# Optimization experiments

Measured on AMD Instinct MI355X. Metric: run time of the kernel, lower is better.

Reference implementation:

```python
import jax, jax.numpy as jnp
import numpy as np

N_NODES = 4096
N_EDGES = 65536
BS = 16
LEAKY_SLOPE = 0.01
BN_EPS = 1e-5


def _init(key, shape, scale=0.02):
    return (jax.random.normal(key, shape, dtype=jnp.float32) * scale)


def setup_inputs() -> dict:
    key = jax.random.key(0)
    ks = jax.random.split(key, 20)
    x_in = jax.random.normal(ks[0], (N_NODES, 8500), dtype=jnp.float32)
    edge_index = jax.random.randint(ks[1], (2, N_EDGES), 0, N_NODES, dtype=jnp.int64)
    return {
        "x_in": x_in,
        "edge_index": edge_index,
        # SAGEConv params: Wl (neighbor lin, with bias), Wr (root lin, no bias)
        "W1l": _init(ks[2], (320, 8500)), "b1": jnp.zeros((320,), jnp.float32), "W1r": _init(ks[3], (320, 8500)),
        "W2l": _init(ks[4], (180, 320)),  "b2": jnp.zeros((180,), jnp.float32), "W2r": _init(ks[5], (180, 320)),
        "W3l": _init(ks[6], (90, 180)),   "b3": jnp.zeros((90,), jnp.float32),  "W3r": _init(ks[7], (90, 180)),
        "W4l": _init(ks[8], (50, 90)),    "b4": jnp.zeros((50,), jnp.float32),  "W4r": _init(ks[9], (50, 90)),
        "Wf1": _init(ks[10], (32, 50)),   "bf1": jnp.zeros((32,), jnp.float32),
        "Wf2": _init(ks[11], (16, 32)),   "bf2": jnp.zeros((16,), jnp.float32),
        "Wf3": _init(ks[12], (1, 16)),    "bf3": jnp.zeros((1,), jnp.float32),
    }


def _sage(x, src, dst, Wl, bl, Wr):
    # PyG SAGEConv: out = lin_l(mean_{j in N(i)} x_j) + lin_r(x_i)
    agg = jax.ops.segment_sum(x[src], dst, num_segments=N_NODES)          # [N, F]
    deg = jax.ops.segment_sum(jnp.ones_like(dst, dtype=x.dtype), dst, num_segments=N_NODES)
    mean = agg / jnp.maximum(deg, 1.0)[:, None]
    return mean @ Wl.T + bl + x @ Wr.T


def _leaky(x):
    return jnp.where(x >= 0, x, LEAKY_SLOPE * x)


def _bn(x):
    # F.batch_norm(x, None, None, training=True): per-feature, biased var, no affine
    m = jnp.mean(x, axis=0)
    v = jnp.mean((x - m) ** 2, axis=0)
    return (x - m) / jnp.sqrt(v + BN_EPS)


def reference(x_in, edge_index,
              W1l, b1, W1r, W2l, b2, W2r, W3l, b3, W3r, W4l, b4, W4r,
              Wf1, bf1, Wf2, bf2, Wf3, bf3):
    src, dst = edge_index[0], edge_index[1]
    x = _bn(_leaky(_sage(x_in, src, dst, W1l, b1, W1r)))
    x = _bn(_leaky(_sage(x, src, dst, W2l, b2, W2r)))
    x = _bn(_leaky(_sage(x, src, dst, W3l, b3, W3r)))
    x = _bn(_leaky(_sage(x, src, dst, W4l, b4, W4r)))
    # get_batch: label i -> floor(i / (N/BS)); global_add_pool == segment sum
    x = x.reshape(BS, N_NODES // BS, -1).sum(axis=1)                      # [BS, 50]
    x = x @ Wf1.T + bf1
    x = x @ Wf2.T + bf2
    x = x @ Wf3.T + bf3
    return x
```

## Files before the change

### kernel.cpp

```cpp
#include <hip/hip_runtime.h>
#include <stdint.h>

#define NN 4096
#define NE 65536
#define LEAKY 0.01f
#define BN_EPS 1e-5f
#define DSTRIDE 96

typedef float f32x4 __attribute__((ext_vector_type(4)));
typedef __bf16 bf16x8 __attribute__((ext_vector_type(8)));
typedef unsigned short u16x8 __attribute__((ext_vector_type(8)));

static __device__ __forceinline__ unsigned short f2bf(float v) {
  unsigned int u = __float_as_uint(v);
  u += 0x7fff + ((u >> 16) & 1);
  return (unsigned short)(u >> 16);
}

typedef __attribute__((address_space(1))) void gvoid;
typedef __attribute__((address_space(3))) void lvoid;

static __device__ __forceinline__ void async16(const void* g, void* l) {
  __builtin_amdgcn_global_load_lds((gvoid*)(uintptr_t)g,
                                   (lvoid*)(uint32_t)(uintptr_t)l, 16, 0, 0);
}


static __device__ __forceinline__ void pack_w_seg(int lblk, const float* __restrict__ Wl,
                                                  const float* __restrict__ Wr,
                                                  unsigned short* __restrict__ dst,
                                                  int Fout, int Fin, int Kp, int Np) {
  int nb = Kp >> 3;
  int idx = lblk * 256 + threadIdx.x;
  if (idx >= Np * nb) return;
  int row = idx / nb, kb = idx - row * nb;
  int g = kb >> 3, b = kb & 7;
  int dkb = (g << 3) | ((b + row) & 7);
  const float* src = nullptr;
  if (row < Fout)          src = Wl + (size_t)row * Fin;
  else if (row < 2 * Fout) src = Wr + (size_t)(row - Fout) * Fin;
  u16x8 st;
#pragma unroll
  for (int o = 0; o < 8; ++o) {
    int k = kb * 8 + o;
    float v = (src && k < Fin) ? src[k] : 0.f;
    st[o] = f2bf(v);
  }
  *(u16x8*)&dst[(size_t)row * Kp + dkb * 8] = st;
}

#define PX_BLK   17024
#define PW1_BLK   2660
#define PW2_BLK     60
#define PW3_BLK     24
#define PW4_BLK      8
#define ADJ_BLK    256
#define SETUP_BLK (PX_BLK + PW1_BLK + PW2_BLK + PW3_BLK + PW4_BLK + ADJ_BLK)

__global__ __launch_bounds__(256) void setup_all(
    const float* __restrict__ x, const int* __restrict__ esrc, const int* __restrict__ edst,
    const float* __restrict__ W1l, const float* __restrict__ W1r,
    const float* __restrict__ W2l, const float* __restrict__ W2r,
    const float* __restrict__ W3l, const float* __restrict__ W3r,
    const float* __restrict__ W4l, const float* __restrict__ W4r,
    unsigned short* __restrict__ xbf, unsigned short* __restrict__ wb1,
    unsigned short* __restrict__ wb2, unsigned short* __restrict__ wb3,
    unsigned short* __restrict__ wb4, int* __restrict__ deg, int* __restrict__ eix) {
  int blk = blockIdx.x;
  if (blk < PX_BLK) {
    int idx = blk * 256 + threadIdx.x;
    int row = idx / 1064, kb = idx - row * 1064;
    int g = kb >> 3, b = kb & 7;
    int dkb = (g << 3) | ((b + row) & 7);
    const float* src = x + (size_t)row * 8500 + kb * 8;
    float v[8];
    if (kb < 1062) {
      f32x4 a = *(const f32x4*)src;
      f32x4 c = *(const f32x4*)(src + 4);
#pragma unroll
      for (int o = 0; o < 4; ++o) { v[o] = a[o]; v[o + 4] = c[o]; }
    } else {
#pragma unroll
      for (int o = 0; o < 8; ++o) {
        int k = kb * 8 + o;
        v[o] = (k < 8500) ? x[(size_t)row * 8500 + k] : 0.f;
      }
    }
    u16x8 st;
#pragma unroll
    for (int o = 0; o < 8; ++o) st[o] = f2bf(v[o]);
    *(u16x8*)&xbf[(size_t)row * 8512 + dkb * 8] = st;
  } else if (blk < PX_BLK + PW1_BLK) {
    pack_w_seg(blk - PX_BLK, W1l, W1r, wb1, 320, 8500, 8512, 640);
  } else if (blk < PX_BLK + PW1_BLK + PW2_BLK) {
    pack_w_seg(blk - PX_BLK - PW1_BLK, W2l, W2r, wb2, 180, 320, 320, 384);
  } else if (blk < PX_BLK + PW1_BLK + PW2_BLK + PW3_BLK) {
    pack_w_seg(blk - PX_BLK - PW1_BLK - PW2_BLK, W3l, W3r, wb3, 90, 180, 192, 256);
  } else if (blk < PX_BLK + PW1_BLK + PW2_BLK + PW3_BLK + PW4_BLK) {
    pack_w_seg(blk - PX_BLK - PW1_BLK - PW2_BLK - PW3_BLK, W4l, W4r, wb4, 50, 90, 128, 128);
  } else {
    int e = (blk - (SETUP_BLK - ADJ_BLK)) * 256 + threadIdx.x;
    int d = edst[e];
    int pos = atomicAdd(&deg[d], 1);
    if (pos < DSTRIDE) eix[(size_t)d * DSTRIDE + pos] = esrc[e];
  }
}

__global__ __launch_bounds__(256) void gemm_bt(const unsigned short* __restrict__ A,
                                               const unsigned short* __restrict__ B,
                                               float* __restrict__ C, int N, int K,
                                               int M) {
  __shared__ unsigned short smem[2 * 128 * 64];
  unsigned short* As = smem;
  unsigned short* Bs = smem + 128 * 64;

  const int t = threadIdx.x;
  const int bm = blockIdx.x, bn = blockIdx.y;
  const int lane = t & 63;
  const int wave = t >> 6;
  const int wm = (wave & 1) * 64, wn = (wave >> 1) * 64;
  const int l16 = lane & 15, quad = lane >> 4;

  const int ksteps = K >> 6;
  const int gz = (int)gridDim.z;
  const int per = (ksteps + gz - 1) / gz;
  const int k0 = (int)blockIdx.z * per;
  int k1 = k0 + per; if (k1 > ksteps) k1 = ksteps;

  f32x4 acc[4][4];
#pragma unroll
  for (int i = 0; i < 4; ++i)
#pragma unroll
    for (int j = 0; j < 4; ++j) acc[i][j] = (f32x4){0.f, 0.f, 0.f, 0.f};

  const int srow = t >> 3;
  const int scol = (t & 7) * 8;
  const unsigned short* Abase = A + (size_t)(bm * 128) * K + scol;
  const unsigned short* Bbase = B + (size_t)(bn * 128) * K + scol;

  for (int kt = k0; kt < k1; ++kt) {
    const unsigned short* Ag = Abase + kt * 64;
    const unsigned short* Bg = Bbase + kt * 64;
#pragma unroll
    for (int p = 0; p < 4; ++p) {
      int row = p * 32 + srow;
      async16(Ag + (size_t)row * K, &As[row * 64 + scol]);
    }
#pragma unroll
    for (int p = 0; p < 4; ++p) {
      int row = p * 32 + srow;
      async16(Bg + (size_t)row * K, &Bs[row * 64 + scol]);
    }
    __syncthreads();
#pragma unroll
    for (int kh = 0; kh < 2; ++kh) {
      const int s8 = ((kh * 4 + quad + l16) & 7) * 8;
      bf16x8 af[4], bfr[4];
#pragma unroll
      for (int i = 0; i < 4; ++i)
        af[i] = *(const bf16x8*)&As[(wm + i * 16 + l16) * 64 + s8];
#pragma unroll
      for (int j = 0; j < 4; ++j)
        bfr[j] = *(const bf16x8*)&Bs[(wn + j * 16 + l16) * 64 + s8];
#pragma unroll
      for (int i = 0; i < 4; ++i)
#pragma unroll
        for (int j = 0; j < 4; ++j)
          acc[i][j] = __builtin_amdgcn_mfma_f32_16x16x32_bf16(af[i], bfr[j], acc[i][j], 0, 0, 0);
    }
    __syncthreads();
  }

  float* Cb = C + (size_t)blockIdx.z * M * N;
#pragma unroll
  for (int i = 0; i < 4; ++i) {
    int rbase = bm * 128 + wm + i * 16 + quad * 4;
#pragma unroll
    for (int j = 0; j < 4; ++j) {
      int col = bn * 128 + wn + j * 16 + l16;
      float* cp = Cb + (size_t)rbase * N + col;
#pragma unroll
      for (int r = 0; r < 4; ++r) cp[(size_t)r * N] = acc[i][j][r];
    }
  }
}

__global__ void reduceN(float* __restrict__ y, int nz) {
  int idx = blockIdx.x * 256 + threadIdx.x;
  f32x4* p = (f32x4*)y;
  const int S = NN * 640 / 4;
  f32x4 v = p[idx];
  for (int sl = 1; sl < nz; ++sl) v += p[idx + (size_t)sl * S];
  p[idx] = v;
}

__global__ __launch_bounds__(256) void sage_agg(
    const float* __restrict__ y, const int* __restrict__ deg,
    const int* __restrict__ eix, const float* __restrict__ bias,
    float* __restrict__ z, int F, int ldy) {
  int i = blockIdx.x;
  int tx = threadIdx.x, ty = threadIdx.y;
  int f4 = (blockIdx.y * 64 + tx) * 4;
  __shared__ int se[DSTRIDE];
  __shared__ float red[3][64][4];
  int d = deg[i]; if (d > DSTRIDE) d = DSTRIDE;
  bool active = (f4 < F);
  f32x4 s = {0.f, 0.f, 0.f, 0.f};
  {
    int lt = ty * 64 + tx;
    if (lt < d) se[lt] = eix[(size_t)i * DSTRIDE + lt];
  }
  __syncthreads();
  if (active)
    for (int e = ty; e < d; e += 4)
      s += *(const f32x4*)&y[(size_t)se[e] * ldy + f4];
  if (ty > 0) *(f32x4*)red[ty - 1][tx] = s;
  __syncthreads();
  if (ty == 0 && active) {
    s += *(const f32x4*)red[0][tx];
    s += *(const f32x4*)red[1][tx];
    s += *(const f32x4*)red[2][tx];
    float inv = 1.f / (float)(d > 1 ? d : 1);
    int cnt = F - f4; if (cnt > 4) cnt = 4;
    const float* yr = &y[(size_t)i * ldy + F + f4];
    float* zo = &z[(size_t)i * F + f4];
    for (int j = 0; j < cnt; ++j) {
      float w = s[j] * inv + yr[j] + bias[f4 + j];
      zo[j] = (w >= 0.f) ? w : LEAKY * w;
    }
  }
}


__global__ __launch_bounds__(256) void bn_part(const float* __restrict__ z,
                                               float* __restrict__ sums, int F) {
  int tx = threadIdx.x, ty = threadIdx.y;
  int f = blockIdx.x * 64 + tx;
  float s = 0.f, s2 = 0.f;
  if (f < F) {
    int r0 = blockIdx.y * 512 + ty * 128;
    for (int j = 0; j < 128; ++j) {
      float v = z[(size_t)(r0 + j) * F + f];
      s += v; s2 += v * v;
    }
  }
  __shared__ float ls[4][64], ls2[4][64];
  ls[ty][tx] = s; ls2[ty][tx] = s2;
  __syncthreads();
  if (ty == 0 && f < F) {
    float S  = ls[0][tx] + ls[1][tx] + ls[2][tx] + ls[3][tx];
    float S2 = ls2[0][tx] + ls2[1][tx] + ls2[2][tx] + ls2[3][tx];
    atomicAdd(&sums[f], S);
    atomicAdd(&sums[F + f], S2);
  }
}

__global__ void bn_norm8(const float* __restrict__ z, const float* __restrict__ sums,
                         unsigned short* __restrict__ xout, int F, int Kp) {
  int nb = Kp >> 3;
  int idx = blockIdx.x * 256 + threadIdx.x;
  int row = idx / nb, kb = idx - row * nb;
  int g = kb >> 3, b = kb & 7;
  int dkb = (g << 3) | ((b + row) & 7);
  u16x8 st;
#pragma unroll
  for (int o = 0; o < 8; ++o) {
    int k = kb * 8 + o;
    float v = 0.f;
    if (k < F) {
      float m  = sums[k] * (1.f / NN);
      float var = sums[F + k] * (1.f / NN) - m * m;
      float rs = rsqrtf(var + BN_EPS);
      v = (z[(size_t)row * F + k] - m) * rs;
    }
    st[o] = f2bf(v);
  }
  *(u16x8*)&xout[(size_t)row * Kp + dkb * 8] = st;
}

__global__ void pool_fc(const float* __restrict__ z,
                        const float* __restrict__ sums,
                        const float* __restrict__ Wf1, const float* __restrict__ bf1,
                        const float* __restrict__ Wf2, const float* __restrict__ bf2,
                        const float* __restrict__ Wf3, const float* __restrict__ bf3,
                        float* __restrict__ out) {
  __shared__ float pool[50];
  __shared__ float h1[32], h2[16];
  int b = blockIdx.x, t = threadIdx.x;
  if (t < 50) {
    float s = 0.f;
    for (int r = 0; r < 256; ++r) s += z[(size_t)(b * 256 + r) * 50 + t];
    float m  = sums[t] * (1.f / NN);
    float var = sums[50 + t] * (1.f / NN) - m * m;
    float rs = rsqrtf(var + BN_EPS);
    pool[t] = (s - 256.f * m) * rs;
  }
  __syncthreads();
  if (t < 32) {
    float s = bf1[t];
    for (int f = 0; f < 50; ++f) s += pool[f] * Wf1[t * 50 + f];
    h1[t] = s;
  }
  __syncthreads();
  if (t < 16) {
    float s = bf2[t];
    for (int f = 0; f < 32; ++f) s += h1[f] * Wf2[t * 32 + f];
    h2[t] = s;
  }
  __syncthreads();
  if (t == 0) {
    float s = bf3[0];
    for (int f = 0; f < 16; ++f) s += h2[f] * Wf3[f];
    out[b] = s;
  }
}


extern "C" void kernel_launch(void* const* d_in, const int* in_sizes, int n_in,
                              void* d_out, int out_size, void* d_ws, size_t ws_size,
                              hipStream_t stream) {
  const float* x_in = (const float*)d_in[0];
  const int* ei = (const int*)d_in[1];
  const float* W1l = (const float*)d_in[2];
  const float* b1  = (const float*)d_in[3];
  const float* W1r = (const float*)d_in[4];
  const float* W2l = (const float*)d_in[5];
  const float* b2  = (const float*)d_in[6];
  const float* W2r = (const float*)d_in[7];
  const float* W3l = (const float*)d_in[8];
  const float* b3  = (const float*)d_in[9];
  const float* W3r = (const float*)d_in[10];
  const float* W4l = (const float*)d_in[11];
  const float* b4  = (const float*)d_in[12];
  const float* W4r = (const float*)d_in[13];
  const float* Wf1 = (const float*)d_in[14];
  const float* bf1 = (const float*)d_in[15];
  const float* Wf2 = (const float*)d_in[16];
  const float* bf2 = (const float*)d_in[17];
  const float* Wf3 = (const float*)d_in[18];
  const float* bf3 = (const float*)d_in[19];
  float* out = (float*)d_out;
  (void)in_sizes; (void)n_in; (void)out_size;

  char* ws = (char*)d_ws;
  size_t off = 0;
  auto alloc = [&](size_t bytes) -> void* {
    void* p = ws + off;
    off = (off + bytes + 255) & ~(size_t)255;
    return p;
  };
  unsigned short* xbf = (unsigned short*)alloc((size_t)NN * 8512 * 2);
  unsigned short* wb1 = (unsigned short*)alloc((size_t)640 * 8512 * 2);
  unsigned short* wb2 = (unsigned short*)alloc((size_t)384 * 320 * 2);
  unsigned short* wb3 = (unsigned short*)alloc((size_t)256 * 192 * 2);
  unsigned short* wb4 = (unsigned short*)alloc((size_t)128 * 128 * 2);
  float* z    = (float*)alloc((size_t)NN * 320 * 4);
  int* deg    = (int*)alloc(NN * 4);
  float* bnsum = (float*)alloc(1280 * 4);
  int* eix    = (int*)alloc((size_t)NN * DSTRIDE * 4);
  const size_t YS = (size_t)NN * 640 * 4;
  float* y = (float*)(ws + off);
  int nz = (off + 8 * YS <= ws_size) ? 8 : 4;
  if (off + (size_t)nz * YS > ws_size) return;
  float* bns1 = bnsum;
  float* bns2 = bnsum + 640;
  float* bns3 = bnsum + 1000;
  float* bns4 = bnsum + 1180;

  hipMemsetAsync(deg, 0, NN * 4 + 1280 * 4, stream);

  setup_all<<<dim3(SETUP_BLK), dim3(256), 0, stream>>>(
      x_in, ei, ei + NE, W1l, W1r, W2l, W2r, W3l, W3r, W4l, W4r,
      xbf, wb1, wb2, wb3, wb4, deg, eix);

  gemm_bt<<<dim3(32, 5, nz), dim3(256), 0, stream>>>(xbf, wb1, y, 640, 8512, NN);
  reduceN<<<dim3(NN * 640 / 4 / 256), dim3(256), 0, stream>>>(y, nz);
  sage_agg<<<dim3(NN, 2), dim3(64, 4), 0, stream>>>(y, deg, eix, b1, z, 320, 640);
  bn_part<<<dim3(5, 8), dim3(64, 4), 0, stream>>>(z, bns1, 320);
  bn_norm8<<<dim3(NN * 40 / 256), dim3(256), 0, stream>>>(z, bns1, xbf, 320, 320);

  gemm_bt<<<dim3(32, 3, 1), dim3(256), 0, stream>>>(xbf, wb2, y, 384, 320, NN);
  sage_agg<<<dim3(NN, 1), dim3(64, 4), 0, stream>>>(y, deg, eix, b2, z, 180, 384);
  bn_part<<<dim3(3, 8), dim3(64, 4), 0, stream>>>(z, bns2, 180);
  bn_norm8<<<dim3(NN * 24 / 256), dim3(256), 0, stream>>>(z, bns2, xbf, 180, 192);

  gemm_bt<<<dim3(32, 2, 1), dim3(256), 0, stream>>>(xbf, wb3, y, 256, 192, NN);
  sage_agg<<<dim3(NN, 1), dim3(64, 4), 0, stream>>>(y, deg, eix, b3, z, 90, 256);
  bn_part<<<dim3(2, 8), dim3(64, 4), 0, stream>>>(z, bns3, 90);
  bn_norm8<<<dim3(NN * 16 / 256), dim3(256), 0, stream>>>(z, bns3, xbf, 90, 128);

  gemm_bt<<<dim3(32, 1, 1), dim3(256), 0, stream>>>(xbf, wb4, y, 128, 128, NN);
  sage_agg<<<dim3(NN, 1), dim3(64, 4), 0, stream>>>(y, deg, eix, b4, z, 50, 128);
  bn_part<<<dim3(1, 8), dim3(64, 4), 0, stream>>>(z, bns4, 50);

  pool_fc<<<dim3(16), dim3(64), 0, stream>>>(z, bns4, Wf1, bf1, Wf2, bf2, Wf3, bf3, out);
}
```

Baseline: 511.8 us.

## Pack 64-element groups per thread, loop feature blocks in sage_agg, fix split-K at 4

The bf16 packing of x and the weights now has each thread load 64 floats and write eight swizzled 16-byte chunks, cutting thread count and index math for the large conversion pass. sage_agg handles all feature blocks in one block per node, with a two-way unrolled gather, so the neighbor list is loaded once instead of once per feature block. The first GEMM's split-K is fixed at 4 instead of 8 when workspace allows, which halves the partial-sum buffers reduceN must read. Risks include higher register pressure from the 64-float arrays, and less parallelism in both the first GEMM and the aggregation.

```diff
diff --git a/kernel.cpp b/kernel.cpp
--- a/kernel.cpp
+++ b/kernel.cpp
@@ -26,36 +26,52 @@
 }
 
 
-static __device__ __forceinline__ void pack_w_seg(int lblk, const float* __restrict__ Wl,
-                                                  const float* __restrict__ Wr,
-                                                  unsigned short* __restrict__ dst,
-                                                  int Fout, int Fin, int Kp, int Np) {
-  int nb = Kp >> 3;
+static __device__ __forceinline__ void pack_w_group(int lblk, const float* __restrict__ Wl,
+                                                    const float* __restrict__ Wr,
+                                                    unsigned short* __restrict__ dst,
+                                                    int Fout, int Fin, int Kp, int Np) {
+  int gpr = Kp >> 6;
   int idx = lblk * 256 + threadIdx.x;
-  if (idx >= Np * nb) return;
-  int row = idx / nb, kb = idx - row * nb;
-  int g = kb >> 3, b = kb & 7;
-  int dkb = (g << 3) | ((b + row) & 7);
+  if (idx >= Np * gpr) return;
+  int row = idx / gpr, g = idx - row * gpr;
   const float* src = nullptr;
   if (row < Fout)          src = Wl + (size_t)row * Fin;
   else if (row < 2 * Fout) src = Wr + (size_t)(row - Fout) * Fin;
-  u16x8 st;
-#pragma unroll
-  for (int o = 0; o < 8; ++o) {
-    int k = kb * 8 + o;
-    float v = (src && k < Fin) ? src[k] : 0.f;
-    st[o] = f2bf(v);
-  }
-  *(u16x8*)&dst[(size_t)row * Kp + dkb * 8] = st;
-}
-
-#define PX_BLK   17024
-#define PW1_BLK   2660
-#define PW2_BLK     60
-#define PW3_BLK     24
-#define PW4_BLK      8
-#define ADJ_BLK    256
-#define SETUP_BLK (PX_BLK + PW1_BLK + PW2_BLK + PW3_BLK + PW4_BLK + ADJ_BLK)
+  float v[64];
+  bool al16 = ((Fin & 3) == 0);
+#pragma unroll
+  for (int vv = 0; vv < 16; ++vv) {
+    int k = g * 64 + vv * 4;
+    f32x4 a = (f32x4){0.f, 0.f, 0.f, 0.f};
+    if (src) {
+      if (al16 && k + 4 <= Fin) {
+        a = *(const f32x4*)(src + k);
+      } else {
+#pragma unroll
+        for (int o = 0; o < 4; ++o) a[o] = (k + o < Fin) ? src[k + o] : 0.f;
+      }
+    }
+#pragma unroll
+    for (int o = 0; o < 4; ++o) v[vv * 4 + o] = a[o];
+  }
+  unsigned short* drow = dst + (size_t)row * Kp;
+#pragma unroll
+  for (int b = 0; b < 8; ++b) {
+    int dkb = (g << 3) | ((b + row) & 7);
+    u16x8 st;
+#pragma unroll
+    for (int o = 0; o < 8; ++o) st[o] = f2bf(v[b * 8 + o]);
+    *(u16x8*)&drow[dkb * 8] = st;
+  }
+}
+
+#define PXG_BLK  2128
+#define PW1G      333
+#define PW2G        8
+#define PW3G        3
+#define PW4G        1
+#define ADJ_BLK   256
+#define SETUP_BLK (PXG_BLK + PW1G + PW2G + PW3G + PW4G + ADJ_BLK)
 
 __global__ __launch_bounds__(256) void setup_all(
     const float* __restrict__ x, const int* __restrict__ esrc, const int* __restrict__ edst,
@@ -67,37 +83,36 @@
     unsigned short* __restrict__ wb2, unsigned short* __restrict__ wb3,
     unsigned short* __restrict__ wb4, int* __restrict__ deg, int* __restrict__ eix) {
   int blk = blockIdx.x;
-  if (blk < PX_BLK) {
+  if (blk < PXG_BLK) {
     int idx = blk * 256 + threadIdx.x;
-    int row = idx / 1064, kb = idx - row * 1064;
-    int g = kb >> 3, b = kb & 7;
-    int dkb = (g << 3) | ((b + row) & 7);
-    const float* src = x + (size_t)row * 8500 + kb * 8;
-    float v[8];
-    if (kb < 1062) {
-      f32x4 a = *(const f32x4*)src;
-      f32x4 c = *(const f32x4*)(src + 4);
-#pragma unroll
-      for (int o = 0; o < 4; ++o) { v[o] = a[o]; v[o + 4] = c[o]; }
-    } else {
-#pragma unroll
-      for (int o = 0; o < 8; ++o) {
-        int k = kb * 8 + o;
-        v[o] = (k < 8500) ? x[(size_t)row * 8500 + k] : 0.f;
-      }
-    }
-    u16x8 st;
-#pragma unroll
-    for (int o = 0; o < 8; ++o) st[o] = f2bf(v[o]);
-    *(u16x8*)&xbf[(size_t)row * 8512 + dkb * 8] = st;
-  } else if (blk < PX_BLK + PW1_BLK) {
-    pack_w_seg(blk - PX_BLK, W1l, W1r, wb1, 320, 8500, 8512, 640);
-  } else if (blk < PX_BLK + PW1_BLK + PW2_BLK) {
-    pack_w_seg(blk - PX_BLK - PW1_BLK, W2l, W2r, wb2, 180, 320, 320, 384);
-  } else if (blk < PX_BLK + PW1_BLK + PW2_BLK + PW3_BLK) {
-    pack_w_seg(blk - PX_BLK - PW1_BLK - PW2_BLK, W3l, W3r, wb3, 90, 180, 192, 256);
-  } else if (blk < PX_BLK + PW1_BLK + PW2_BLK + PW3_BLK + PW4_BLK) {
-    pack_w_seg(blk - PX_BLK - PW1_BLK - PW2_BLK - PW3_BLK, W4l, W4r, wb4, 50, 90, 128, 128);
+    int row = idx / 133, g = idx - row * 133;
+    const float* xrow = x + (size_t)row * 8500;
+    float v[64];
+#pragma unroll
+    for (int vv = 0; vv < 16; ++vv) {
+      int k = g * 64 + vv * 4;
+      f32x4 a = (k + 4 <= 8500) ? *(const f32x4*)(xrow + k)
+                                : (f32x4){0.f, 0.f, 0.f, 0.f};
+#pragma unroll
+      for (int o = 0; o < 4; ++o) v[vv * 4 + o] = a[o];
+    }
+    unsigned short* drow = xbf + (size_t)row * 8512;
+#pragma unroll
+    for (int b = 0; b < 8; ++b) {
+      int dkb = (g << 3) | ((b + row) & 7);
+      u16x8 st;
+#pragma unroll
+      for (int o = 0; o < 8; ++o) st[o] = f2bf(v[b * 8 + o]);
+      *(u16x8*)&drow[dkb * 8] = st;
+    }
+  } else if (blk < PXG_BLK + PW1G) {
+    pack_w_group(blk - PXG_BLK, W1l, W1r, wb1, 320, 8500, 8512, 640);
+  } else if (blk < PXG_BLK + PW1G + PW2G) {
+    pack_w_group(blk - PXG_BLK - PW1G, W2l, W2r, wb2, 180, 320, 320, 384);
+  } else if (blk < PXG_BLK + PW1G + PW2G + PW3G) {
+    pack_w_group(blk - PXG_BLK - PW1G - PW2G, W3l, W3r, wb3, 90, 180, 192, 256);
+  } else if (blk < PXG_BLK + PW1G + PW2G + PW3G + PW4G) {
+    pack_w_group(blk - PXG_BLK - PW1G - PW2G - PW3G, W4l, W4r, wb4, 50, 90, 128, 128);
   } else {
     int e = (blk - (SETUP_BLK - ADJ_BLK)) * 256 + threadIdx.x;
     int d = edst[e];
@@ -200,34 +215,45 @@
     float* __restrict__ z, int F, int ldy) {
   int i = blockIdx.x;
   int tx = threadIdx.x, ty = threadIdx.y;
-  int f4 = (blockIdx.y * 64 + tx) * 4;
   __shared__ int se[DSTRIDE];
   __shared__ float red[3][64][4];
   int d = deg[i]; if (d > DSTRIDE) d = DSTRIDE;
-  bool active = (f4 < F);
-  f32x4 s = {0.f, 0.f, 0.f, 0.f};
   {
     int lt = ty * 64 + tx;
     if (lt < d) se[lt] = eix[(size_t)i * DSTRIDE + lt];
   }
   __syncthreads();
-  if (active)
-    for (int e = ty; e < d; e += 4)
-      s += *(const f32x4*)&y[(size_t)se[e] * ldy + f4];
-  if (ty > 0) *(f32x4*)red[ty - 1][tx] = s;
-  __syncthreads();
-  if (ty == 0 && active) {
-    s += *(const f32x4*)red[0][tx];
-    s += *(const f32x4*)red[1][tx];
-    s += *(const f32x4*)red[2][tx];
-    float inv = 1.f / (float)(d > 1 ? d : 1);
-    int cnt = F - f4; if (cnt > 4) cnt = 4;
-    const float* yr = &y[(size_t)i * ldy + F + f4];
-    float* zo = &z[(size_t)i * F + f4];
-    for (int j = 0; j < cnt; ++j) {
-      float w = s[j] * inv + yr[j] + bias[f4 + j];
-      zo[j] = (w >= 0.f) ? w : LEAKY * w;
-    }
+  int nfb = (F + 255) >> 8;
+  for (int fb = 0; fb < nfb; ++fb) {
+    int f4 = (fb * 64 + tx) * 4;
+    bool active = (f4 < F);
+    f32x4 s = {0.f, 0.f, 0.f, 0.f};
+    if (active) {
+      const float* yb = y + f4;
+      int e = ty;
+      for (; e + 4 < d; e += 8) {
+        f32x4 a = *(const f32x4*)&yb[(size_t)se[e] * ldy];
+        f32x4 b = *(const f32x4*)&yb[(size_t)se[e + 4] * ldy];
+        s += a; s += b;
+      }
+      if (e < d) s += *(const f32x4*)&yb[(size_t)se[e] * ldy];
+    }
+    if (ty > 0) *(f32x4*)red[ty - 1][tx] = s;
+    __syncthreads();
+    if (ty == 0 && active) {
+      s += *(const f32x4*)red[0][tx];
+      s += *(const f32x4*)red[1][tx];
+      s += *(const f32x4*)red[2][tx];
+      float inv = 1.f / (float)(d > 1 ? d : 1);
+      int cnt = F - f4; if (cnt > 4) cnt = 4;
+      const float* yr = &y[(size_t)i * ldy + F + f4];
+      float* zo = &z[(size_t)i * F + f4];
+      for (int j = 0; j < cnt; ++j) {
+        float w = s[j] * inv + yr[j] + bias[f4 + j];
+        zo[j] = (w >= 0.f) ? w : LEAKY * w;
+      }
+    }
+    if (fb + 1 < nfb) __syncthreads();
   }
 }
 
@@ -360,7 +386,7 @@
   int* eix    = (int*)alloc((size_t)NN * DSTRIDE * 4);
   const size_t YS = (size_t)NN * 640 * 4;
   float* y = (float*)(ws + off);
-  int nz = (off + 8 * YS <= ws_size) ? 8 : 4;
+  const int nz = 4;
   if (off + (size_t)nz * YS > ws_size) return;
   float* bns1 = bnsum;
   float* bns2 = bnsum + 640;
@@ -375,22 +401,22 @@
 
   gemm_bt<<<dim3(32, 5, nz), dim3(256), 0, stream>>>(xbf, wb1, y, 640, 8512, NN);
   reduceN<<<dim3(NN * 640 / 4 / 256), dim3(256), 0, stream>>>(y, nz);
-  sage_agg<<<dim3(NN, 2), dim3(64, 4), 0, stream>>>(y, deg, eix, b1, z, 320, 640);
+  sage_agg<<<dim3(NN), dim3(64, 4), 0, stream>>>(y, deg, eix, b1, z, 320, 640);
   bn_part<<<dim3(5, 8), dim3(64, 4), 0, stream>>>(z, bns1, 320);
   bn_norm8<<<dim3(NN * 40 / 256), dim3(256), 0, stream>>>(z, bns1, xbf, 320, 320);
 
   gemm_bt<<<dim3(32, 3, 1), dim3(256), 0, stream>>>(xbf, wb2, y, 384, 320, NN);
-  sage_agg<<<dim3(NN, 1), dim3(64, 4), 0, stream>>>(y, deg, eix, b2, z, 180, 384);
+  sage_agg<<<dim3(NN), dim3(64, 4), 0, stream>>>(y, deg, eix, b2, z, 180, 384);
   bn_part<<<dim3(3, 8), dim3(64, 4), 0, stream>>>(z, bns2, 180);
   bn_norm8<<<dim3(NN * 24 / 256), dim3(256), 0, stream>>>(z, bns2, xbf, 180, 192);
 
   gemm_bt<<<dim3(32, 2, 1), dim3(256), 0, stream>>>(xbf, wb3, y, 256, 192, NN);
-  sage_agg<<<dim3(NN, 1), dim3(64, 4), 0, stream>>>(y, deg, eix, b3, z, 90, 256);
+  sage_agg<<<dim3(NN), dim3(64, 4), 0, stream>>>(y, deg, eix, b3, z, 90, 256);
   bn_part<<<dim3(2, 8), dim3(64, 4), 0, stream>>>(z, bns3, 90);
   bn_norm8<<<dim3(NN * 16 / 256), dim3(256), 0, stream>>>(z, bns3, xbf, 90, 128);
 
   gemm_bt<<<dim3(32, 1, 1), dim3(256), 0, stream>>>(xbf, wb4, y, 128, 128, NN);
-  sage_agg<<<dim3(NN, 1), dim3(64, 4), 0, stream>>>(y, deg, eix, b4, z, 50, 128);
+  sage_agg<<<dim3(NN), dim3(64, 4), 0, stream>>>(y, deg, eix, b4, z, 50, 128);
   bn_part<<<dim3(1, 8), dim3(64, 4), 0, stream>>>(z, bns4, 50);
 
   pool_fc<<<dim3(16), dim3(64), 0, stream>>>(z, bns4, Wf1, bf1, Wf2, bf2, Wf3, bf3, out);
```

Measured after the change: 519.1 us. Within noise of the previous version (+1.4%).

## Batch setup conversions, loop feature blocks in aggregation, and fix split-K at four

Applied to the files above, without the earlier changes.

The x-to-bf16 conversion now handles two chunks per thread, so the setup kernel launches half as many of those blocks, and the adjacency-building blocks move to the front so their atomics start early. sage_agg loops over feature blocks inside one block per node instead of using a 2D grid, which loads each node's neighbour list once. Its gather loop is unrolled by two to keep more loads in flight. The split-K depth of the first GEMM is fixed at 4 instead of 8 when workspace allows, which halves the partial buffers and the reduceN traffic but gives the large GEMM fewer blocks to run in parallel.

```diff
diff --git a/kernel.cpp b/kernel.cpp
--- a/kernel.cpp
+++ b/kernel.cpp
@@ -49,13 +49,43 @@
   *(u16x8*)&dst[(size_t)row * Kp + dkb * 8] = st;
 }
 
-#define PX_BLK   17024
-#define PW1_BLK   2660
-#define PW2_BLK     60
-#define PW3_BLK     24
-#define PW4_BLK      8
+static __device__ __forceinline__ void px_load(const float* __restrict__ x, int idx,
+                                               float v[8]) {
+  int row = idx / 1064, kb = idx - row * 1064;
+  const float* src = x + (size_t)row * 8500 + kb * 8;
+  if (kb < 1062) {
+    f32x4 a = *(const f32x4*)src;
+    f32x4 c = *(const f32x4*)(src + 4);
+#pragma unroll
+    for (int o = 0; o < 4; ++o) { v[o] = a[o]; v[o + 4] = c[o]; }
+  } else {
+#pragma unroll
+    for (int o = 0; o < 8; ++o) {
+      int k = kb * 8 + o;
+      v[o] = (k < 8500) ? src[o] : 0.f;
+    }
+  }
+}
+
+static __device__ __forceinline__ void px_store(unsigned short* __restrict__ xbf, int idx,
+                                                const float v[8]) {
+  int row = idx / 1064, kb = idx - row * 1064;
+  int g = kb >> 3, b = kb & 7;
+  int dkb = (g << 3) | ((b + row) & 7);
+  u16x8 st;
+#pragma unroll
+  for (int o = 0; o < 8; ++o) st[o] = f2bf(v[o]);
+  *(u16x8*)&xbf[(size_t)row * 8512 + dkb * 8] = st;
+}
+
 #define ADJ_BLK    256
-#define SETUP_BLK (PX_BLK + PW1_BLK + PW2_BLK + PW3_BLK + PW4_BLK + ADJ_BLK)
+#define PX_HALF  2179072
+#define PX_BLK     8512
+#define PW1_BLK    2660
+#define PW2_BLK      60
+#define PW3_BLK      24
+#define PW4_BLK       8
+#define SETUP_BLK (ADJ_BLK + PX_BLK + PW1_BLK + PW2_BLK + PW3_BLK + PW4_BLK)
 
 __global__ __launch_bounds__(256) void setup_all(
     const float* __restrict__ x, const int* __restrict__ esrc, const int* __restrict__ edst,
@@ -67,42 +97,28 @@
     unsigned short* __restrict__ wb2, unsigned short* __restrict__ wb3,
     unsigned short* __restrict__ wb4, int* __restrict__ deg, int* __restrict__ eix) {
   int blk = blockIdx.x;
-  if (blk < PX_BLK) {
-    int idx = blk * 256 + threadIdx.x;
-    int row = idx / 1064, kb = idx - row * 1064;
-    int g = kb >> 3, b = kb & 7;
-    int dkb = (g << 3) | ((b + row) & 7);
-    const float* src = x + (size_t)row * 8500 + kb * 8;
-    float v[8];
-    if (kb < 1062) {
-      f32x4 a = *(const f32x4*)src;
-      f32x4 c = *(const f32x4*)(src + 4);
-#pragma unroll
-      for (int o = 0; o < 4; ++o) { v[o] = a[o]; v[o + 4] = c[o]; }
-    } else {
-#pragma unroll
-      for (int o = 0; o < 8; ++o) {
-        int k = kb * 8 + o;
-        v[o] = (k < 8500) ? x[(size_t)row * 8500 + k] : 0.f;
-      }
-    }
-    u16x8 st;
-#pragma unroll
-    for (int o = 0; o < 8; ++o) st[o] = f2bf(v[o]);
-    *(u16x8*)&xbf[(size_t)row * 8512 + dkb * 8] = st;
-  } else if (blk < PX_BLK + PW1_BLK) {
-    pack_w_seg(blk - PX_BLK, W1l, W1r, wb1, 320, 8500, 8512, 640);
-  } else if (blk < PX_BLK + PW1_BLK + PW2_BLK) {
-    pack_w_seg(blk - PX_BLK - PW1_BLK, W2l, W2r, wb2, 180, 320, 320, 384);
-  } else if (blk < PX_BLK + PW1_BLK + PW2_BLK + PW3_BLK) {
-    pack_w_seg(blk - PX_BLK - PW1_BLK - PW2_BLK, W3l, W3r, wb3, 90, 180, 192, 256);
-  } else if (blk < PX_BLK + PW1_BLK + PW2_BLK + PW3_BLK + PW4_BLK) {
-    pack_w_seg(blk - PX_BLK - PW1_BLK - PW2_BLK - PW3_BLK, W4l, W4r, wb4, 50, 90, 128, 128);
-  } else {
-    int e = (blk - (SETUP_BLK - ADJ_BLK)) * 256 + threadIdx.x;
+  if (blk < ADJ_BLK) {
+    int e = blk * 256 + threadIdx.x;
     int d = edst[e];
     int pos = atomicAdd(&deg[d], 1);
     if (pos < DSTRIDE) eix[(size_t)d * DSTRIDE + pos] = esrc[e];
+  } else if (blk < ADJ_BLK + PX_BLK) {
+    int idx0 = (blk - ADJ_BLK) * 256 + threadIdx.x;
+    int idx1 = idx0 + PX_HALF;
+    float v0[8], v1[8];
+    px_load(x, idx0, v0);
+    px_load(x, idx1, v1);
+    px_store(xbf, idx0, v0);
+    px_store(xbf, idx1, v1);
+  } else if (blk < ADJ_BLK + PX_BLK + PW1_BLK) {
+    pack_w_seg(blk - ADJ_BLK - PX_BLK, W1l, W1r, wb1, 320, 8500, 8512, 640);
+  } else if (blk < ADJ_BLK + PX_BLK + PW1_BLK + PW2_BLK) {
+    pack_w_seg(blk - ADJ_BLK - PX_BLK - PW1_BLK, W2l, W2r, wb2, 180, 320, 320, 384);
+  } else if (blk < ADJ_BLK + PX_BLK + PW1_BLK + PW2_BLK + PW3_BLK) {
+    pack_w_seg(blk - ADJ_BLK - PX_BLK - PW1_BLK - PW2_BLK, W3l, W3r, wb3, 90, 180, 192, 256);
+  } else {
+    pack_w_seg(blk - ADJ_BLK - PX_BLK - PW1_BLK - PW2_BLK - PW3_BLK, W4l, W4r, wb4,
+               50, 90, 128, 128);
   }
 }
 
@@ -200,34 +216,45 @@
     float* __restrict__ z, int F, int ldy) {
   int i = blockIdx.x;
   int tx = threadIdx.x, ty = threadIdx.y;
-  int f4 = (blockIdx.y * 64 + tx) * 4;
   __shared__ int se[DSTRIDE];
   __shared__ float red[3][64][4];
   int d = deg[i]; if (d > DSTRIDE) d = DSTRIDE;
-  bool active = (f4 < F);
-  f32x4 s = {0.f, 0.f, 0.f, 0.f};
   {
     int lt = ty * 64 + tx;
     if (lt < d) se[lt] = eix[(size_t)i * DSTRIDE + lt];
   }
   __syncthreads();
-  if (active)
-    for (int e = ty; e < d; e += 4)
-      s += *(const f32x4*)&y[(size_t)se[e] * ldy + f4];
-  if (ty > 0) *(f32x4*)red[ty - 1][tx] = s;
-  __syncthreads();
-  if (ty == 0 && active) {
-    s += *(const f32x4*)red[0][tx];
-    s += *(const f32x4*)red[1][tx];
-    s += *(const f32x4*)red[2][tx];
-    float inv = 1.f / (float)(d > 1 ? d : 1);
-    int cnt = F - f4; if (cnt > 4) cnt = 4;
-    const float* yr = &y[(size_t)i * ldy + F + f4];
-    float* zo = &z[(size_t)i * F + f4];
-    for (int j = 0; j < cnt; ++j) {
-      float w = s[j] * inv + yr[j] + bias[f4 + j];
-      zo[j] = (w >= 0.f) ? w : LEAKY * w;
-    }
+  int nfb = (F + 255) >> 8;
+  for (int fb = 0; fb < nfb; ++fb) {
+    int f4 = (fb * 64 + tx) * 4;
+    bool active = (f4 < F);
+    f32x4 s = {0.f, 0.f, 0.f, 0.f};
+    if (active) {
+      const float* yb = y + f4;
+      int e = ty;
+      for (; e + 4 < d; e += 8) {
+        f32x4 a = *(const f32x4*)&yb[(size_t)se[e] * ldy];
+        f32x4 b = *(const f32x4*)&yb[(size_t)se[e + 4] * ldy];
+        s += a; s += b;
+      }
+      if (e < d) s += *(const f32x4*)&yb[(size_t)se[e] * ldy];
+    }
+    if (ty > 0) *(f32x4*)red[ty - 1][tx] = s;
+    __syncthreads();
+    if (ty == 0 && active) {
+      s += *(const f32x4*)red[0][tx];
+      s += *(const f32x4*)red[1][tx];
+      s += *(const f32x4*)red[2][tx];
+      float inv = 1.f / (float)(d > 1 ? d : 1);
+      int cnt = F - f4; if (cnt > 4) cnt = 4;
+      const float* yr = &y[(size_t)i * ldy + F + f4];
+      float* zo = &z[(size_t)i * F + f4];
+      for (int j = 0; j < cnt; ++j) {
+        float w = s[j] * inv + yr[j] + bias[f4 + j];
+        zo[j] = (w >= 0.f) ? w : LEAKY * w;
+      }
+    }
+    if (fb + 1 < nfb) __syncthreads();
   }
 }
 
@@ -360,7 +387,7 @@
   int* eix    = (int*)alloc((size_t)NN * DSTRIDE * 4);
   const size_t YS = (size_t)NN * 640 * 4;
   float* y = (float*)(ws + off);
-  int nz = (off + 8 * YS <= ws_size) ? 8 : 4;
+  const int nz = 4;
   if (off + (size_t)nz * YS > ws_size) return;
   float* bns1 = bnsum;
   float* bns2 = bnsum + 640;
@@ -375,22 +402,22 @@
 
   gemm_bt<<<dim3(32, 5, nz), dim3(256), 0, stream>>>(xbf, wb1, y, 640, 8512, NN);
   reduceN<<<dim3(NN * 640 / 4 / 256), dim3(256), 0, stream>>>(y, nz);
-  sage_agg<<<dim3(NN, 2), dim3(64, 4), 0, stream>>>(y, deg, eix, b1, z, 320, 640);
+  sage_agg<<<dim3(NN), dim3(64, 4), 0, stream>>>(y, deg, eix, b1, z, 320, 640);
   bn_part<<<dim3(5, 8), dim3(64, 4), 0, stream>>>(z, bns1, 320);
   bn_norm8<<<dim3(NN * 40 / 256), dim3(256), 0, stream>>>(z, bns1, xbf, 320, 320);
 
   gemm_bt<<<dim3(32, 3, 1), dim3(256), 0, stream>>>(xbf, wb2, y, 384, 320, NN);
-  sage_agg<<<dim3(NN, 1), dim3(64, 4), 0, stream>>>(y, deg, eix, b2, z, 180, 384);
+  sage_agg<<<dim3(NN), dim3(64, 4), 0, stream>>>(y, deg, eix, b2, z, 180, 384);
   bn_part<<<dim3(3, 8), dim3(64, 4), 0, stream>>>(z, bns2, 180);
   bn_norm8<<<dim3(NN * 24 / 256), dim3(256), 0, stream>>>(z, bns2, xbf, 180, 192);
 
   gemm_bt<<<dim3(32, 2, 1), dim3(256), 0, stream>>>(xbf, wb3, y, 256, 192, NN);
-  sage_agg<<<dim3(NN, 1), dim3(64, 4), 0, stream>>>(y, deg, eix, b3, z, 90, 256);
+  sage_agg<<<dim3(NN), dim3(64, 4), 0, stream>>>(y, deg, eix, b3, z, 90, 256);
   bn_part<<<dim3(2, 8), dim3(64, 4), 0, stream>>>(z, bns3, 90);
   bn_norm8<<<dim3(NN * 16 / 256), dim3(256), 0, stream>>>(z, bns3, xbf, 90, 128);
 
   gemm_bt<<<dim3(32, 1, 1), dim3(256), 0, stream>>>(xbf, wb4, y, 128, 128, NN);
-  sage_agg<<<dim3(NN, 1), dim3(64, 4), 0, stream>>>(y, deg, eix, b4, z, 50, 128);
+  sage_agg<<<dim3(NN), dim3(64, 4), 0, stream>>>(y, deg, eix, b4, z, 50, 128);
   bn_part<<<dim3(1, 8), dim3(64, 4), 0, stream>>>(z, bns4, 50);
 
   pool_fc<<<dim3(16), dim3(64), 0, stream>>>(z, bns4, Wf1, bf1, Wf2, bf2, Wf3, bf3, out);
```

Measured after the change: 505.5 us. Within noise of the previous version (-1.2%).
